# Optimization experiments

Measured on AMD Instinct MI355X. Metric: run time of the kernel, lower is better.

Reference implementation:

```python
import jax, jax.numpy as jnp
import numpy as np
import math

B, S, D = 16, 1024, 2048  # batch, seq_len, feats_size; LSTM hidden H = D
H = D

def setup_inputs() -> dict:
    key = jax.random.key(0)
    ks = jax.random.split(key, 12)
    s = 1.0 / math.sqrt(D)
    return {
        "feats": jax.random.normal(ks[0], (B, S, D), jnp.float32),
        "Wq": jax.random.normal(ks[1], (D, D), jnp.float32) * s,
        "bq": jnp.zeros((D,), jnp.float32),
        "Wk": jax.random.normal(ks[2], (D, D), jnp.float32) * s,
        "bk": jnp.zeros((D,), jnp.float32),
        "Wv": jax.random.normal(ks[3], (D, D), jnp.float32) * s,
        "bv": jnp.zeros((D,), jnp.float32),
        "W_ih": jax.random.normal(ks[4], (4 * H, D), jnp.float32) * s,
        "W_hh": jax.random.normal(ks[5], (4 * H, H), jnp.float32) * s,
        "b_ih": jnp.zeros((4 * H,), jnp.float32),
        "b_hh": jnp.zeros((4 * H,), jnp.float32),
    }

def _lstm(x, W_ih, W_hh, b_ih, b_hh):
    # x: [B, S, D] -> hidden sequence [B, S, H]. torch nn.LSTM gate order i,f,g,o.
    xg = jnp.einsum('bsd,gd->bsg', x, W_ih) + b_ih + b_hh  # [B,S,4H], input part precomputed
    xg = jnp.swapaxes(xg, 0, 1)  # [S,B,4H] for scan over time
    h0 = jnp.zeros((x.shape[0], H), x.dtype)
    c0 = jnp.zeros((x.shape[0], H), x.dtype)
    def step(carry, xt):
        h, c = carry
        gates = xt + h @ W_hh.T  # [B,4H]
        i, f, g, o = jnp.split(gates, 4, axis=-1)
        c = jax.nn.sigmoid(f) * c + jax.nn.sigmoid(i) * jnp.tanh(g)
        h = jax.nn.sigmoid(o) * jnp.tanh(c)
        return (h, c), h
    _, hs = jax.lax.scan(step, (h0, c0), xg)
    return jnp.swapaxes(hs, 0, 1)  # [B,S,H]

def reference(feats, Wq, bq, Wk, bk, Wv, bv, W_ih, W_hh, b_ih, b_hh):
    q = feats @ Wq.T + bq
    k = feats @ Wk.T + bk
    v = feats @ Wv.T + bv
    dot = jnp.einsum('bsd,btd->bst', q, k) / math.sqrt(2048.0)
    w = jax.nn.softmax(dot, axis=-1)
    new_feats = jnp.einsum('bst,btd->bsd', w, v)
    return _lstm(new_feats, W_ih, W_hh, b_ih, b_hh)
```

## Files before the change

kernel.cpp:

```cpp
#include <hip/hip_runtime.h>


typedef unsigned short u16;
typedef unsigned int u32;
typedef unsigned long long u64;
typedef __attribute__((ext_vector_type(8))) __bf16 bf16x8;
typedef __attribute__((ext_vector_type(8))) unsigned short u16x8;
typedef __attribute__((ext_vector_type(4))) float f32x4;
typedef __attribute__((ext_vector_type(4))) unsigned int u32x4;

#define DEV static __device__ __forceinline__

DEV u16 f2bf(float f) {
  union { float f; unsigned u; } x; x.f = f;
  return (u16)((x.u + 0x7FFFu + ((x.u >> 16) & 1u)) >> 16);
}
DEV float bf2f(u16 h) {
  union { unsigned u; float f; } x; x.u = (unsigned)h << 16;
  return x.f;
}
DEV void gload_lds16(const void* g, void* l) {
  __builtin_amdgcn_global_load_lds(
      (const __attribute__((address_space(1))) unsigned int*)g,
      (__attribute__((address_space(3))) unsigned int*)l, 16, 0, 0);
}

__global__ __launch_bounds__(256) void k_cvt(const float* __restrict__ in,
                                             u16* __restrict__ out, long n) {
  long i = (((long)blockIdx.x << 8) | threadIdx.x) << 3;
  if (i >= n) return;
  float4 f0 = *(const float4*)(in + i);
  float4 f1 = *(const float4*)(in + i + 4);
  u16x8 p;
  p[0] = f2bf(f0.x); p[1] = f2bf(f0.y); p[2] = f2bf(f0.z); p[3] = f2bf(f0.w);
  p[4] = f2bf(f1.x); p[5] = f2bf(f1.y); p[6] = f2bf(f1.z); p[7] = f2bf(f1.w);
  *(u16x8*)(out + i) = p;
}

__global__ __launch_bounds__(256) void k_addb(const float* __restrict__ a,
                                              const float* __restrict__ b,
                                              float* __restrict__ o, int n) {
  int i = blockIdx.x * 256 + threadIdx.x;
  if (i < n) o[i] = a[i] + b[i];
}

template<int OBF>
__global__ __launch_bounds__(256) void k_gemm_nt(
    const u16* __restrict__ A, const u16* __restrict__ B, void* __restrict__ Cv,
    const float* __restrict__ bias, float scale, int M, int N, int K,
    long sA, long sB, long sC) {
  __shared__ __attribute__((aligned(16))) u16 As[4096];
  __shared__ __attribute__((aligned(16))) u16 Bs[4096];
  const int tid = threadIdx.x;
  const int lane = tid & 63;
  const int wm = ((tid >> 7) & 1) * 64;
  const int wn = ((tid >> 6) & 1) * 64;
  const int gx = gridDim.x;
  int lin = blockIdx.y * gx + blockIdx.x;
  const int nwg = gx * gridDim.y;
  if ((nwg & 7) == 0) lin = (lin & 7) * (nwg >> 3) + (lin >> 3);
  const long bm = (long)(lin / gx) << 7;
  const long bn = (long)(lin % gx) << 7;
  const u16* Ab = A + (long)blockIdx.z * sA;
  const u16* Bb = B + (long)blockIdx.z * sB;
  const int srow = tid >> 2, scol = (tid & 3) << 3;
  const u16* ga0 = Ab + (bm + srow) * (long)K + scol;
  const u16* gb0 = Bb + (bn + srow) * (long)K + scol;
  const long k64 = (long)K << 6;
  char* lA = (char*)As + tid * 16;
  char* lB = (char*)Bs + tid * 16;
  f32x4 acc[4][4] = {};
  const int fr = lane & 15, fk = (lane >> 4) << 3;
  for (int kt = 0; kt < K; kt += 32) {
    gload_lds16(ga0 + kt, lA);
    gload_lds16(ga0 + k64 + kt, lA + 4096);
    gload_lds16(gb0 + kt, lB);
    gload_lds16(gb0 + k64 + kt, lB + 4096);
    __syncthreads();
    bf16x8 av[4], bv[4];
#pragma unroll
    for (int x = 0; x < 4; ++x) {
      av[x] = *(const bf16x8*)&As[(wm + x * 16 + fr) * 32 + fk];
      bv[x] = *(const bf16x8*)&Bs[(wn + x * 16 + fr) * 32 + fk];
    }
#pragma unroll
    for (int i = 0; i < 4; ++i)
#pragma unroll
      for (int j = 0; j < 4; ++j)
        acc[i][j] = __builtin_amdgcn_mfma_f32_16x16x32_bf16(av[i], bv[j], acc[i][j], 0, 0, 0);
    __syncthreads();
  }
  const long cb = (long)blockIdx.z * sC;
#pragma unroll
  for (int j = 0; j < 4; ++j) {
    const long col = bn + wn + j * 16 + fr;
    const float bb = bias ? bias[col] : 0.f;
#pragma unroll
    for (int i = 0; i < 4; ++i) {
      const long r0 = bm + wm + i * 16 + ((lane >> 4) << 2);
#pragma unroll
      for (int r = 0; r < 4; ++r) {
        const float v = acc[i][j][r] * scale + bb;
        const long off = cb + (r0 + r) * (long)N + col;
        if (OBF) ((u16*)Cv)[off] = f2bf(v);
        else     ((float*)Cv)[off] = v;
      }
    }
  }
}

__global__ __launch_bounds__(256) void k_softmax(const float* __restrict__ S,
                                                 u16* __restrict__ P) {
  __shared__ float red[8];
  const long row = blockIdx.x;
  const float* sr = S + (row << 10);
  const int t = threadIdx.x, lane = t & 63, w = t >> 6;
  float v0 = sr[t], v1 = sr[t + 256], v2 = sr[t + 512], v3 = sr[t + 768];
  float m = fmaxf(fmaxf(v0, v1), fmaxf(v2, v3));
#pragma unroll
  for (int o = 32; o; o >>= 1) m = fmaxf(m, __shfl_xor(m, o));
  if (lane == 0) red[w] = m;
  __syncthreads();
  m = fmaxf(fmaxf(red[0], red[1]), fmaxf(red[2], red[3]));
  v0 = __expf(v0 - m); v1 = __expf(v1 - m); v2 = __expf(v2 - m); v3 = __expf(v3 - m);
  float s = v0 + v1 + v2 + v3;
#pragma unroll
  for (int o = 32; o; o >>= 1) s += __shfl_xor(s, o);
  if (lane == 0) red[4 + w] = s;
  __syncthreads();
  s = red[4] + red[5] + red[6] + red[7];
  const float rs = 1.f / s;
  u16* pr = P + (row << 10);
  pr[t] = f2bf(v0 * rs); pr[t + 256] = f2bf(v1 * rs);
  pr[t + 512] = f2bf(v2 * rs); pr[t + 768] = f2bf(v3 * rs);
}

__global__ __launch_bounds__(256) void k_transpose(const u16* __restrict__ V,
                                                   u16* __restrict__ VT) {
  __shared__ __attribute__((aligned(16))) u16 tile[64][80];
  const long b = blockIdx.z;
  const long t0 = (long)blockIdx.y << 6, d0 = (long)blockIdx.x << 6;
  const int r = threadIdx.x >> 3, c8 = (threadIdx.x & 7) << 3;
  const u16* src = V + ((b << 10) + t0) * 2048 + d0;
#pragma unroll
  for (int p = 0; p < 2; ++p) {
    const int rr = r + p * 32;
    *(u16x8*)&tile[rr][c8] = *(const u16x8*)(src + (long)rr * 2048 + c8);
  }
  __syncthreads();
  u16* dst = VT + ((b << 11) + d0) * 1024 + t0;
#pragma unroll
  for (int p = 0; p < 2; ++p) {
    const int dr = r + p * 32;
    u16x8 pk;
#pragma unroll
    for (int q = 0; q < 8; ++q) pk[q] = tile[c8 + q][dr];
    *(u16x8*)(dst + (long)dr * 1024 + c8) = pk;
  }
}

DEV bf16x8 wread(const char* wlds, int nrow, int k) {
  int byte = (nrow << 12) + (k << 1);
  byte ^= (nrow & 7) << 4;
  return *(const bf16x8*)(wlds + byte);
}
DEV float sigm(float x) { return 1.f / (1.f + __expf(-x)); }
DEV float tanh_fast(float x) { return 1.f - 2.f / (1.f + __expf(2.f * x)); }

__global__ __launch_bounds__(256, 1) void k_lstm(
    const u16* __restrict__ xg, const u16* __restrict__ whh,
    u16* __restrict__ hbuf, float* __restrict__ out,
    unsigned* __restrict__ flg) {
  extern __shared__ char smem[];
  char* wlds = smem;
  float* red = (float*)(smem + 131072);
  const int tid = threadIdx.x, lane = tid & 63, wave = tid >> 6;
  const int j0 = blockIdx.x << 4;
  const int am = lane & 15, ak = (lane >> 4) << 3;
  const int bb = tid >> 4, jj = tid & 15;

  for (int it = 0; it < 32; ++it) {
    const long grow = ((long)(it >> 4) << 11) + j0 + (it & 15);
    const u16* src = whh + grow * 2048 + (tid << 3);
    int byte = (it << 12) + (tid << 4);
    byte ^= (it & 7) << 4;
    *(bf16x8*)(wlds + byte) = *(const bf16x8*)src;
  }
  bf16x8 wf[2][16];
#pragma unroll
  for (int g2 = 0; g2 < 2; ++g2)
#pragma unroll
    for (int ks = 0; ks < 16; ++ks)
      wf[g2][ks] = *(const bf16x8*)(whh + ((long)((2 + g2) << 11) + j0 + am) * 2048 +
                                    (wave << 9) + (ks << 5) + ak);
  __syncthreads();

  float c = 0.f;
  unsigned* const myflag = flg + (((wave << 5) + (lane & 31)) << 2);
  u16 xv[4];
#pragma unroll
  for (int g = 0; g < 4; ++g)
    xv[g] = xg[((long)bb << 10) * 8192 + (g << 11) + j0 + jj];

  for (int t = 0; t < 1024; ++t) {
    const int par = t & 1;
    unsigned dep = 0;
    if (t) {
      const unsigned tgt = (unsigned)t;
      unsigned v = tgt;
      for (;;) {
        if (lane < 32)
          v = __hip_atomic_load(myflag, __ATOMIC_RELAXED, __HIP_MEMORY_SCOPE_AGENT);
        if (__all(v >= tgt)) break;
        __builtin_amdgcn_s_sleep(1);
      }
      dep = v >> 20;
    }
    asm volatile("" : "+v"(dep)::);

    const u16* hbase = hbuf + ((par ^ 1) << 15);
    const u32 voff = ((am << 11) + (wave << 9) + ak + dep) << 1;
    u32x4 hd[16];
#define HLD(I, OFF)                                                          \
    asm volatile("global_load_dwordx4 %0, %1, %2 offset:" #OFF " sc0 sc1"    \
                 : "=v"(hd[I]) : "v"(voff), "s"(hbase));
    HLD(0, 0)    HLD(1, 64)   HLD(2, 128)  HLD(3, 192)
    HLD(4, 256)  HLD(5, 320)  HLD(6, 384)  HLD(7, 448)
    HLD(8, 512)  HLD(9, 576)  HLD(10, 640) HLD(11, 704)
    HLD(12, 768) HLD(13, 832) HLD(14, 896) HLD(15, 960)
#undef HLD
    asm volatile("s_waitcnt vmcnt(0)" ::: "memory");
    __builtin_amdgcn_sched_barrier(0);

    f32x4 a0 = {0.f, 0.f, 0.f, 0.f}, a1 = a0, a2 = a0, a3 = a0;
#pragma unroll
    for (int ks = 0; ks < 16; ++ks) {
      union { u32x4 d; bf16x8 v; } u;
      u.d = hd[ks];
      const int k = (wave << 9) + (ks << 5) + ak;
      a0 = __builtin_amdgcn_mfma_f32_16x16x32_bf16(u.v, wread(wlds, am, k),      a0, 0, 0, 0);
      a1 = __builtin_amdgcn_mfma_f32_16x16x32_bf16(u.v, wread(wlds, am + 16, k), a1, 0, 0, 0);
      a2 = __builtin_amdgcn_mfma_f32_16x16x32_bf16(u.v, wf[0][ks], a2, 0, 0, 0);
      a3 = __builtin_amdgcn_mfma_f32_16x16x32_bf16(u.v, wf[1][ks], a3, 0, 0, 0);
    }
    {
      float* rw = red + (wave << 10);
      const int mrow = (lane >> 4) << 2;
#pragma unroll
      for (int r = 0; r < 4; ++r) {
        rw[(mrow + r) * 64 + am]      = a0[r];
        rw[(mrow + r) * 64 + 16 + am] = a1[r];
        rw[(mrow + r) * 64 + 32 + am] = a2[r];
        rw[(mrow + r) * 64 + 48 + am] = a3[r];
      }
    }
    __syncthreads();
    float g4[4];
#pragma unroll
    for (int g = 0; g < 4; ++g) {
      const int n = (bb << 6) + (g << 4) + jj;
      g4[g] = red[n] + red[1024 + n] + red[2048 + n] + red[3072 + n] + bf2f(xv[g]);
    }
    const float gi = sigm(g4[0]);
    const float gf = sigm(g4[1]);
    const float gg = tanh_fast(g4[2]);
    const float go = sigm(g4[3]);
    c = gf * c + gi * gg;
    const float h = go * tanh_fast(c);
    {
      const unsigned hb = (unsigned)f2bf(h);
      const unsigned p1 = (unsigned)__shfl_xor((int)hb, 1);
      const unsigned w2 = (hb & 0xFFFFu) | (p1 << 16);
      const unsigned p2 = (unsigned)__shfl_xor((int)w2, 2);
      if ((jj & 3) == 0) {
        const u64 hw = (u64)w2 | ((u64)p2 << 32);
        u16* dst = hbuf + (par << 15) + (bb << 11) + j0 + jj;
        __hip_atomic_store((u64*)dst, hw, __ATOMIC_RELAXED, __HIP_MEMORY_SCOPE_AGENT);
      }
    }
    asm volatile("s_waitcnt vmcnt(0)" ::: "memory");
    __syncthreads();
    if (tid == 0)
      __hip_atomic_store(flg + (blockIdx.x << 2), (unsigned)(t + 1),
                         __ATOMIC_RELAXED, __HIP_MEMORY_SCOPE_AGENT);
    out[(((long)(bb << 10) + t) << 11) + j0 + jj] = h;
    {
      const int tn = (t + 1 < 1024) ? t + 1 : 0;
#pragma unroll
      for (int g = 0; g < 4; ++g)
        xv[g] = xg[((long)((bb << 10) + tn)) * 8192 + (g << 11) + j0 + jj];
    }
    asm volatile("" ::: "memory");
  }
}

extern "C" void kernel_launch(void* const* d_in, const int* in_sizes, int n_in,
                              void* d_out, int out_size, void* d_ws, size_t ws_size,
                              hipStream_t stream) {
  const float* feats = (const float*)d_in[0];
  const float* Wq = (const float*)d_in[1];
  const float* bq = (const float*)d_in[2];
  const float* Wk = (const float*)d_in[3];
  const float* bk = (const float*)d_in[4];
  const float* Wv = (const float*)d_in[5];
  const float* bv = (const float*)d_in[6];
  const float* Wih = (const float*)d_in[7];
  const float* Whh = (const float*)d_in[8];
  const float* bih = (const float*)d_in[9];
  const float* bhh = (const float*)d_in[10];
  float* out = (float*)d_out;
  char* ws = (char*)d_ws;

  u16* feats16 = (u16*)(ws + 0L);
  u16* q16     = (u16*)(ws + 67108864L);
  u16* k16     = (u16*)(ws + 134217728L);
  u16* v16     = (u16*)(ws + 201326592L);
  u16* vT16    = feats16;
  u16* P16     = q16;
  u16* xg16    = (u16*)(ws + 0L);
  u16* nf16    = (u16*)(ws + 268435456L);
  u16* wq16    = (u16*)(ws + 335544320L);
  u16* wk16    = (u16*)(ws + 343932928L);
  u16* wv16    = (u16*)(ws + 352321536L);
  u16* wih16   = (u16*)(ws + 360710144L);
  u16* whh16   = (u16*)(ws + 394264576L);
  float* biassum = (float*)(ws + 427819008L);
  u16* hbuf    = (u16*)(ws + 427851776L);
  unsigned* flg = (unsigned*)(ws + 427982848L);
  float* scoresf = (float*)d_out;

  k_cvt<<<16384, 256, 0, stream>>>(feats, feats16, 33554432L);
  k_cvt<<<2048, 256, 0, stream>>>(Wq, wq16, 4194304L);
  k_cvt<<<2048, 256, 0, stream>>>(Wk, wk16, 4194304L);
  k_cvt<<<2048, 256, 0, stream>>>(Wv, wv16, 4194304L);
  k_cvt<<<8192, 256, 0, stream>>>(Wih, wih16, 16777216L);
  k_cvt<<<8192, 256, 0, stream>>>(Whh, whh16, 16777216L);
  k_addb<<<32, 256, 0, stream>>>(bih, bhh, biassum, 8192);

  k_gemm_nt<1><<<dim3(16, 128, 1), 256, 0, stream>>>(feats16, wq16, q16, bq, 1.f, 16384, 2048, 2048, 0, 0, 0);
  k_gemm_nt<1><<<dim3(16, 128, 1), 256, 0, stream>>>(feats16, wk16, k16, bk, 1.f, 16384, 2048, 2048, 0, 0, 0);
  k_gemm_nt<1><<<dim3(16, 128, 1), 256, 0, stream>>>(feats16, wv16, v16, bv, 1.f, 16384, 2048, 2048, 0, 0, 0);
  k_gemm_nt<0><<<dim3(8, 8, 16), 256, 0, stream>>>(q16, k16, scoresf, nullptr, 0.022097086912079608f,
                                                   1024, 1024, 2048, 2097152, 2097152, 1048576);
  k_softmax<<<16384, 256, 0, stream>>>(scoresf, P16);
  k_transpose<<<dim3(32, 16, 16), 256, 0, stream>>>(v16, vT16);
  k_gemm_nt<1><<<dim3(16, 8, 16), 256, 0, stream>>>(P16, vT16, nf16, nullptr, 1.f,
                                                    1024, 2048, 1024, 1048576, 2097152, 2097152);
  k_gemm_nt<1><<<dim3(64, 128, 1), 256, 0, stream>>>(nf16, wih16, xg16, biassum, 1.f, 16384, 8192, 2048, 0, 0, 0);

  hipMemsetAsync(ws + 427851776L, 0, 131072 + 4096, stream);
  const int dynlds = 131072 + 16384;
  (void)hipFuncSetAttribute((const void*)k_lstm, hipFuncAttributeMaxDynamicSharedMemorySize, dynlds);
  void* kargs[] = {(void*)&xg16, (void*)&whh16, (void*)&hbuf, (void*)&out, (void*)&flg};
  hipError_t ce = hipLaunchCooperativeKernel((const void*)k_lstm, dim3(128), dim3(256),
                                             kargs, dynlds, stream);
  if (ce != hipSuccess) {
    k_lstm<<<dim3(128), dim3(256), dynlds, stream>>>(xg16, whh16, hbuf, out, flg);
  }
}
```

Measured before the change: 7.084 ms.

## Add 256x256-tile 4-stage pipelined bf16 GEMM for QKV and input projections

Introduces a new 512-thread GEMM kernel with 256x256 output tiles, a 4-deep LDS ring of direct global-to-LDS loads, XOR-swizzled LDS layout, and grouped workgroup remapping. It replaces the generic 128-tile GEMM for the Q/K/V projections and the LSTM input projection. Larger tiles raise arithmetic intensity and reduce global traffic. The 128KB LDS footprint limits occupancy to one block per CU, and the kernel assumes dimensions divisible by 256.

```diff
diff --git a/kernel.cpp b/kernel.cpp
--- a/kernel.cpp
+++ b/kernel.cpp
@@ -109,6 +109,113 @@
   }
 }
 
+__global__ __launch_bounds__(512, 2) void k_gemm256(
+    const u16* __restrict__ A, const u16* __restrict__ B,
+    u16* __restrict__ C, const float* __restrict__ bias, int N, int K) {
+  extern __shared__ u16 lds[];
+  u16* As = lds;
+  u16* Bs = lds + 32768;
+  const int tid = threadIdx.x;
+  const int lane = tid & 63, wid = tid >> 6;
+  const int wm = (wid >> 2) & 1, wn = wid & 3;
+  const int gx = gridDim.x;
+  int lin = blockIdx.y * gx + blockIdx.x;
+  const int nwg = gx * gridDim.y;
+  if ((nwg & 7) == 0) lin = (lin & 7) * (nwg >> 3) + (lin >> 3);
+  const long bm = (long)(lin / gx) << 8;
+  const long bn = (long)(lin % gx) << 8;
+  const int NK = K >> 5;
+
+  u32 srow[2], scolb[2];
+#pragma unroll
+  for (int p = 0; p < 2; ++p) {
+    const u32 q = (u32)(p * 8192 + tid * 16);
+    const u32 qp = q ^ (((q >> 9) & 1u) << 5);
+    srow[p] = qp >> 6; scolb[p] = qp & 63u;
+  }
+#define STAGE256(S, KT)                                                      \
+  {                                                                          \
+    _Pragma("unroll")                                                        \
+    for (int p = 0; p < 2; ++p) {                                            \
+      const u32 q = (u32)(p * 8192 + tid * 16);                              \
+      gload_lds16(A + (bm + srow[p]) * (long)K + (KT) * 32 + (scolb[p] >> 1),\
+                  (char*)As + (S) * 16384 + q);                              \
+      gload_lds16(B + (bn + srow[p]) * (long)K + (KT) * 32 + (scolb[p] >> 1),\
+                  (char*)Bs + (S) * 16384 + q);                              \
+    }                                                                        \
+  }
+
+  const int fr = lane & 15, fkb = ((lane >> 4) << 3) << 1;
+  u32 abyte[8], bbyte[4];
+#pragma unroll
+  for (int mi = 0; mi < 8; ++mi) {
+    const u32 row = (u32)(wm * 128 + mi * 16 + fr);
+    abyte[mi] = (row * 64 + (u32)fkb) ^ ((row & 8u) ? 32u : 0u);
+  }
+#pragma unroll
+  for (int ni = 0; ni < 4; ++ni) {
+    const u32 row = (u32)(wn * 64 + ni * 16 + fr);
+    bbyte[ni] = (row * 64 + (u32)fkb) ^ ((row & 8u) ? 32u : 0u);
+  }
+
+  f32x4 acc[8][4] = {};
+#define COMPUTE256(SLOT)                                                     \
+  {                                                                          \
+    const char* sa = (const char*)As + (SLOT) * 16384;                       \
+    const char* sb = (const char*)Bs + (SLOT) * 16384;                       \
+    bf16x8 av[8], bv[4];                                                     \
+    _Pragma("unroll")                                                        \
+    for (int mi = 0; mi < 8; ++mi) av[mi] = *(const bf16x8*)(sa + abyte[mi]);\
+    _Pragma("unroll")                                                        \
+    for (int ni = 0; ni < 4; ++ni) bv[ni] = *(const bf16x8*)(sb + bbyte[ni]);\
+    asm volatile("s_waitcnt lgkmcnt(0)" ::: "memory");                       \
+    __builtin_amdgcn_s_barrier();                                            \
+    __builtin_amdgcn_s_setprio(1);                                           \
+    _Pragma("unroll")                                                        \
+    for (int mi = 0; mi < 8; ++mi)                                           \
+      _Pragma("unroll")                                                      \
+      for (int ni = 0; ni < 4; ++ni)                                         \
+        acc[mi][ni] = __builtin_amdgcn_mfma_f32_16x16x32_bf16(               \
+            av[mi], bv[ni], acc[mi][ni], 0, 0, 0);                           \
+    __builtin_amdgcn_s_setprio(0);                                           \
+  }
+
+  STAGE256(0, 0)
+  STAGE256(1, 1)
+  STAGE256(2, 2)
+  int kt = 0;
+  for (; kt < NK - 3; ++kt) {
+    STAGE256((kt + 3) & 3, kt + 3)
+    asm volatile("s_waitcnt vmcnt(12)" ::: "memory");
+    __builtin_amdgcn_s_barrier();
+    COMPUTE256(kt & 3)
+  }
+  asm volatile("s_waitcnt vmcnt(8)" ::: "memory");
+  __builtin_amdgcn_s_barrier();
+  COMPUTE256(kt & 3) ++kt;
+  asm volatile("s_waitcnt vmcnt(4)" ::: "memory");
+  __builtin_amdgcn_s_barrier();
+  COMPUTE256(kt & 3) ++kt;
+  asm volatile("s_waitcnt vmcnt(0)" ::: "memory");
+  __builtin_amdgcn_s_barrier();
+  COMPUTE256(kt & 3)
+#undef STAGE256
+#undef COMPUTE256
+
+#pragma unroll
+  for (int ni = 0; ni < 4; ++ni) {
+    const long col = bn + wn * 64 + ni * 16 + fr;
+    const float bb = bias ? bias[col] : 0.f;
+#pragma unroll
+    for (int mi = 0; mi < 8; ++mi) {
+      const long r0 = bm + wm * 128 + mi * 16 + ((lane >> 4) << 2);
+#pragma unroll
+      for (int r = 0; r < 4; ++r)
+        C[(r0 + r) * (long)N + col] = f2bf(acc[mi][ni][r] + bb);
+    }
+  }
+}
+
 __global__ __launch_bounds__(256) void k_softmax(const float* __restrict__ S,
                                                  u16* __restrict__ P) {
   __shared__ float red[8];
@@ -337,16 +444,17 @@
   k_cvt<<<8192, 256, 0, stream>>>(Whh, whh16, 16777216L);
   k_addb<<<32, 256, 0, stream>>>(bih, bhh, biassum, 8192);
 
-  k_gemm_nt<1><<<dim3(16, 128, 1), 256, 0, stream>>>(feats16, wq16, q16, bq, 1.f, 16384, 2048, 2048, 0, 0, 0);
-  k_gemm_nt<1><<<dim3(16, 128, 1), 256, 0, stream>>>(feats16, wk16, k16, bk, 1.f, 16384, 2048, 2048, 0, 0, 0);
-  k_gemm_nt<1><<<dim3(16, 128, 1), 256, 0, stream>>>(feats16, wv16, v16, bv, 1.f, 16384, 2048, 2048, 0, 0, 0);
+  (void)hipFuncSetAttribute((const void*)k_gemm256, hipFuncAttributeMaxDynamicSharedMemorySize, 131072);
+  k_gemm256<<<dim3(8, 64), 512, 131072, stream>>>(feats16, wq16, q16, bq, 2048, 2048);
+  k_gemm256<<<dim3(8, 64), 512, 131072, stream>>>(feats16, wk16, k16, bk, 2048, 2048);
+  k_gemm256<<<dim3(8, 64), 512, 131072, stream>>>(feats16, wv16, v16, bv, 2048, 2048);
   k_gemm_nt<0><<<dim3(8, 8, 16), 256, 0, stream>>>(q16, k16, scoresf, nullptr, 0.022097086912079608f,
                                                    1024, 1024, 2048, 2097152, 2097152, 1048576);
   k_softmax<<<16384, 256, 0, stream>>>(scoresf, P16);
   k_transpose<<<dim3(32, 16, 16), 256, 0, stream>>>(v16, vT16);
   k_gemm_nt<1><<<dim3(16, 8, 16), 256, 0, stream>>>(P16, vT16, nf16, nullptr, 1.f,
                                                     1024, 2048, 1024, 1048576, 2097152, 2097152);
-  k_gemm_nt<1><<<dim3(64, 128, 1), 256, 0, stream>>>(nf16, wih16, xg16, biassum, 1.f, 16384, 8192, 2048, 0, 0, 0);
+  k_gemm256<<<dim3(32, 64), 512, 131072, stream>>>(nf16, wih16, xg16, biassum, 8192, 2048);
 
   hipMemsetAsync(ws + 427851776L, 0, 131072 + 4096, stream);
   const int dynlds = 131072 + 16384;
```

New measurement: 6.779 ms. 1.05x faster.
